# Kernel optimization log

Measured on AMD Instinct MI355X. Metric: run time of the kernel, lower is better.

## Reference

```python
import jax, jax.numpy as jnp
import numpy as np

B, C, N, F = 256, 4, 64, 256   # batch, in_channels, neighbors, in_features
OC, OF = 8, 256                # out_channels, out_features


def setup_inputs() -> dict:
    key = jax.random.key(0)
    k1, k2, k3, k4, k5 = jax.random.split(key, 5)
    x = jax.random.normal(k1, (B, C, F), dtype=jnp.float32)
    neighbor = jax.random.normal(k2, (B, N, C, F), dtype=jnp.float32)
    # torch.nn.Linear weights are (out_features, in_features)
    W_att1 = jax.random.normal(k3, (C, F), dtype=jnp.float32) / np.sqrt(F).astype(np.float32)
    W_att2 = jax.random.normal(k4, (C, F), dtype=jnp.float32) / np.sqrt(F).astype(np.float32)
    # Conv1d weight: (out_c*out_f, 2C, F); kernel_size==F makes it a dense contraction
    W_conv = jax.random.normal(k5, (OC * OF, 2 * C, F), dtype=jnp.float32) / np.sqrt(2 * C * F).astype(np.float32)
    return {"x": x, "neighbor": neighbor, "W_att1": W_att1, "W_att2": W_att2, "W_conv": W_conv}


def reference(x, neighbor, W_att1, W_att2, W_conv):
    # --- attention weights: einsum 'ci,nkl->n' = sum(att1(x_i)) * sum_{k,l} att2(y_i)[n]
    s1 = jnp.sum(x @ W_att1.T, axis=(1, 2))              # (B,)
    s2 = jnp.sum(neighbor @ W_att2.T, axis=(2, 3))       # (B, N)
    w = jax.nn.softmax(s1[:, None] * s2, axis=1)         # softmax over neighbors (dim 0 per-sample)

    # --- feature adjacency: einsum 'ca,ncb,n->cab' vectorized over batch
    fadj = jnp.einsum('bcx,bncy,bn->bcxy', x, neighbor, w)   # (B, C, F, F)
    fadj = fadj + jnp.swapaxes(fadj, -1, -2)
    # sgnroot
    fadj = jnp.sign(fadj) * jnp.sqrt(jnp.clip(jnp.abs(fadj), 1e-8, None))
    # row normalize over dim -2, NaN -> 0
    adj = fadj / (jnp.abs(fadj).sum(axis=-2, keepdims=True) + 1e-7)
    adj = jnp.where(jnp.isnan(adj), jnp.float32(0.0), adj)

    # --- transform: cat([adj @ x, x], channel) then full-width conv1d (dense contraction)
    h = jnp.einsum('bcxy,bcy->bcx', adj, x)              # (B, C, F)
    z = jnp.concatenate([h, x], axis=1)                  # (B, 2C, F)
    out = jnp.einsum('bcf,ocf->bo', z, W_conv).reshape(B, OC, OF)
    return out, adj
```

## Files before the change

### kernel.cpp

```cpp
#include <hip/hip_runtime.h>
#include <hip/hip_bf16.h>
#include <math.h>


typedef __bf16 bf16x8 __attribute__((ext_vector_type(8)));
typedef __bf16 bf16x4 __attribute__((ext_vector_type(4)));
typedef float f32x4 __attribute__((ext_vector_type(4)));

#define NB 256
#define NC 4
#define NN 64
#define NF 256
#define NO 2048

__global__ __launch_bounds__(256) void k_pre(
    const float* __restrict__ x, const float* __restrict__ nb,
    const float* __restrict__ W1, const float* __restrict__ W2,
    const float* __restrict__ Wc,
    __hip_bfloat16* __restrict__ Wcb, __hip_bfloat16* __restrict__ zbf,
    float* __restrict__ s1, float* __restrict__ s2)
{
  __shared__ float w2s[256], w1s[256];
  int t = threadIdx.x;
  int w = t >> 6, l = t & 63;

  w2s[t] = W2[t] + W2[256 + t] + W2[512 + t] + W2[768 + t];
  w1s[t] = W1[t] + W1[256 + t] + W1[512 + t] + W1[768 + t];
  __syncthreads();

  int gw = blockIdx.x * 4 + w;
  float4 wv2 = *(const float4*)&w2s[l * 4];
  float4 wv1 = *(const float4*)&w1s[l * 4];
  for (int task = gw; task < 16640; task += 8192) {
    bool isS2 = task < 16384;
    const float4* src = isS2 ? ((const float4*)nb + (size_t)task * 256)
                             : ((const float4*)x + (size_t)(task - 16384) * 256);
    float4 wv = isS2 ? wv2 : wv1;
    float val = 0.f;
    #pragma unroll
    for (int k = 0; k < 4; ++k) {
      float4 v = src[l + 64 * k];
      val += v.x * wv.x + v.y * wv.y + v.z * wv.z + v.w * wv.w;
    }
    for (int off = 32; off > 0; off >>= 1) val += __shfl_down(val, off);
    if (l == 0) {
      if (isS2) s2[task] = val;
      else s1[task - 16384] = val;
    }
  }

  for (int task = blockIdx.x; task < 4352; task += 2048) {
    if (task < 4096) {
      int idx = task * 256 + t;
      float4 v = ((const float4*)Wc)[idx];
      bf16x4 o = { (__bf16)v.x, (__bf16)v.y, (__bf16)v.z, (__bf16)v.w };
      ((bf16x4*)Wcb)[idx] = o;
    } else {
      int i = (task - 4096) * 256 + t;
      int e = i * 4;
      int b = e >> 10, r = e & 1023;
      float4 v = ((const float4*)x)[i];
      bf16x4 o = { (__bf16)v.x, (__bf16)v.y, (__bf16)v.z, (__bf16)v.w };
      *(bf16x4*)(zbf + (size_t)b * 2048 + 1024 + r) = o;
    }
  }
}

__global__ __launch_bounds__(256) void k_adj(
    const float* __restrict__ x, const float* __restrict__ nb,
    const float* __restrict__ s1, const float* __restrict__ s2,
    float* __restrict__ adj, __hip_bfloat16* __restrict__ zbf)
{
  __shared__ float xs[256], ns[256], invs[256], wsh[64];
  __shared__ float part[4][256];
  int t = threadIdx.x;
  int w = t >> 6, l = t & 63;
  int blk = blockIdx.x;
  int b = blk >> 2, c = blk & 3;

  if (t < 64) {
    float v = s1[b] * s2[b * 64 + t];
    float m = v;
    for (int off = 32; off > 0; off >>= 1) m = fmaxf(m, __shfl_xor(m, off));
    float e = expf(v - m);
    float s = e;
    for (int off = 32; off > 0; off >>= 1) s += __shfl_xor(s, off);
    wsh[t] = e / s;
  }
  xs[t] = x[(size_t)blk * 256 + t];
  __syncthreads();

  const float4* nb4 = (const float4*)(nb + (size_t)b * 65536 + c * 256);
  float4 a4 = {0.f, 0.f, 0.f, 0.f};
  #pragma unroll
  for (int k = 0; k < 16; ++k) {
    int n = w + 4 * k;
    float4 v = nb4[(size_t)n * 256 + l];
    float wn = wsh[n];
    a4.x = fmaf(wn, v.x, a4.x);
    a4.y = fmaf(wn, v.y, a4.y);
    a4.z = fmaf(wn, v.z, a4.z);
    a4.w = fmaf(wn, v.w, a4.w);
  }
  *(float4*)&part[w][l * 4] = a4;
  __syncthreads();
  ns[t] = part[0][t] + part[1][t] + part[2][t] + part[3][t];
  __syncthreads();

  int j0 = l * 4;
  float4 xv = *(const float4*)&xs[j0];
  float4 nv = *(const float4*)&ns[j0];
  int i0 = w * 64;

  float4 cs = {0.f, 0.f, 0.f, 0.f};
  #pragma unroll 4
  for (int ii = 0; ii < 64; ++ii) {
    int i = i0 + ii;
    float xi = xs[i], ni = ns[i];
    cs.x += __builtin_amdgcn_sqrtf(fmaxf(fabsf(fmaf(xi, nv.x, xv.x * ni)), 1e-8f));
    cs.y += __builtin_amdgcn_sqrtf(fmaxf(fabsf(fmaf(xi, nv.y, xv.y * ni)), 1e-8f));
    cs.z += __builtin_amdgcn_sqrtf(fmaxf(fabsf(fmaf(xi, nv.z, xv.z * ni)), 1e-8f));
    cs.w += __builtin_amdgcn_sqrtf(fmaxf(fabsf(fmaf(xi, nv.w, xv.w * ni)), 1e-8f));
  }
  *(float4*)&part[w][j0] = cs;
  __syncthreads();
  invs[t] = 1.f / (part[0][t] + part[1][t] + part[2][t] + part[3][t] + 1e-7f);
  __syncthreads();

  float4 iv = *(const float4*)&invs[j0];
  float4 ha = {0.f, 0.f, 0.f, 0.f};
  float* ab = adj + (size_t)blk * 65536;
  #pragma unroll 4
  for (int ii = 0; ii < 64; ++ii) {
    int i = i0 + ii;
    float xi = xs[i], ni = ns[i];
    float pix = invs[i] * xi;
    float v0 = fmaf(xi, nv.x, xv.x * ni);
    float v1 = fmaf(xi, nv.y, xv.y * ni);
    float v2 = fmaf(xi, nv.z, xv.z * ni);
    float v3 = fmaf(xi, nv.w, xv.w * ni);
    float g0 = copysignf(__builtin_amdgcn_sqrtf(fmaxf(fabsf(v0), 1e-8f)), v0);
    float g1 = copysignf(__builtin_amdgcn_sqrtf(fmaxf(fabsf(v1), 1e-8f)), v1);
    float g2 = copysignf(__builtin_amdgcn_sqrtf(fmaxf(fabsf(v2), 1e-8f)), v2);
    float g3 = copysignf(__builtin_amdgcn_sqrtf(fmaxf(fabsf(v3), 1e-8f)), v3);
    f32x4 o = { g0 * iv.x, g1 * iv.y, g2 * iv.z, g3 * iv.w };
    __builtin_nontemporal_store(o, (f32x4*)&ab[(size_t)i * 256 + j0]);
    ha.x = fmaf(g0, pix, ha.x);
    ha.y = fmaf(g1, pix, ha.y);
    ha.z = fmaf(g2, pix, ha.z);
    ha.w = fmaf(g3, pix, ha.w);
  }
  __syncthreads();
  *(float4*)&part[w][j0] = ha;
  __syncthreads();
  float hsum = part[0][t] + part[1][t] + part[2][t] + part[3][t];
  zbf[(size_t)b * 2048 + c * 256 + t] = __float2bfloat16(hsum);
}

__global__ __launch_bounds__(256) void k_gemm(
    const __hip_bfloat16* __restrict__ zb, const __hip_bfloat16* __restrict__ Wcb,
    float* __restrict__ out)
{
  int tid = threadIdx.x;
  int wave = tid >> 6, lane = tid & 63;
  int g = lane >> 4, r = lane & 15;
  int bm = blockIdx.x & 7, bn = blockIdx.x >> 3;
  int m0 = bm * 32 + (wave & 1) * 16;
  int n0 = bn * 32 + (wave >> 1) * 16;

  const bf16x8* pa = (const bf16x8*)(zb  + (size_t)(m0 + r) * 2048 + g * 8);
  const bf16x8* pw = (const bf16x8*)(Wcb + (size_t)(n0 + r) * 2048 + g * 8);

  f32x4 acc0 = {0.f, 0.f, 0.f, 0.f}, acc1 = {0.f, 0.f, 0.f, 0.f};
  #pragma unroll 4
  for (int ks = 0; ks < 64; ks += 2) {
    bf16x8 a0 = pa[ks * 4];
    bf16x8 b0 = pw[ks * 4];
    bf16x8 a1 = pa[ks * 4 + 4];
    bf16x8 b1 = pw[ks * 4 + 4];
    acc0 = __builtin_amdgcn_mfma_f32_16x16x32_bf16(a0, b0, acc0, 0, 0, 0);
    acc1 = __builtin_amdgcn_mfma_f32_16x16x32_bf16(a1, b1, acc1, 0, 0, 0);
  }
  acc0 += acc1;
  #pragma unroll
  for (int q = 0; q < 4; ++q) {
    int row = m0 + g * 4 + q;
    __builtin_nontemporal_store(acc0[q], &out[(size_t)row * 2048 + n0 + r]);
  }
}

__global__ __launch_bounds__(256) void k_scores_fb(
    const float* __restrict__ x, const float* __restrict__ nb,
    const float* __restrict__ W1, const float* __restrict__ W2,
    float* __restrict__ s1, float* __restrict__ s2)
{
  __shared__ float red[4];
  int t = threadIdx.x;
  int gid = blockIdx.x;
  float val;
  if (gid < NB * NN) {
    float w = W2[t] + W2[256 + t] + W2[512 + t] + W2[768 + t];
    const float* p = nb + (size_t)gid * 1024;
    val = w * (p[t] + p[256 + t] + p[512 + t] + p[768 + t]);
  } else {
    int b = gid - NB * NN;
    float w = W1[t] + W1[256 + t] + W1[512 + t] + W1[768 + t];
    const float* p = x + (size_t)b * 1024;
    val = w * (p[t] + p[256 + t] + p[512 + t] + p[768 + t]);
  }
  for (int off = 32; off > 0; off >>= 1) val += __shfl_down(val, off);
  if ((t & 63) == 0) red[t >> 6] = val;
  __syncthreads();
  if (t == 0) {
    float s = red[0] + red[1] + red[2] + red[3];
    if (gid < NB * NN) s2[gid] = s;
    else s1[gid - NB * NN] = s;
  }
}

__global__ __launch_bounds__(256) void k_adj_fb(
    const float* __restrict__ x, const float* __restrict__ nb,
    const float* __restrict__ s1, const float* __restrict__ s2,
    float* __restrict__ adj, float* __restrict__ hf)
{
  __shared__ float xs[256], ns[256], invs[256], wsh[64];
  __shared__ float part[4][256];
  int t = threadIdx.x;
  int w = t >> 6, l = t & 63;
  int blk = blockIdx.x;
  int b = blk >> 2, c = blk & 3;

  if (t < 64) {
    float v = s1[b] * s2[b * 64 + t];
    float m = v;
    for (int off = 32; off > 0; off >>= 1) m = fmaxf(m, __shfl_xor(m, off));
    float e = expf(v - m);
    float s = e;
    for (int off = 32; off > 0; off >>= 1) s += __shfl_xor(s, off);
    wsh[t] = e / s;
  }
  __syncthreads();
  float acc = 0.f;
  const float* pb = nb + (size_t)b * 65536 + c * 256 + t;
  #pragma unroll 8
  for (int n = 0; n < 64; ++n) acc = fmaf(wsh[n], pb[(size_t)n * 1024], acc);
  ns[t] = acc;
  xs[t] = x[(size_t)blk * 256 + t];
  __syncthreads();

  int j0 = l * 4;
  float4 xv = *(const float4*)&xs[j0];
  float4 nv = *(const float4*)&ns[j0];
  int i0 = w * 64;
  float4 cs = {0.f, 0.f, 0.f, 0.f};
  for (int ii = 0; ii < 64; ++ii) {
    int i = i0 + ii;
    float xi = xs[i], ni = ns[i];
    cs.x += __builtin_amdgcn_sqrtf(fmaxf(fabsf(fmaf(xi, nv.x, xv.x * ni)), 1e-8f));
    cs.y += __builtin_amdgcn_sqrtf(fmaxf(fabsf(fmaf(xi, nv.y, xv.y * ni)), 1e-8f));
    cs.z += __builtin_amdgcn_sqrtf(fmaxf(fabsf(fmaf(xi, nv.z, xv.z * ni)), 1e-8f));
    cs.w += __builtin_amdgcn_sqrtf(fmaxf(fabsf(fmaf(xi, nv.w, xv.w * ni)), 1e-8f));
  }
  *(float4*)&part[w][j0] = cs;
  __syncthreads();
  invs[t] = 1.f / (part[0][t] + part[1][t] + part[2][t] + part[3][t] + 1e-7f);
  __syncthreads();

  float4 iv = *(const float4*)&invs[j0];
  float4 ha = {0.f, 0.f, 0.f, 0.f};
  float* ab = adj + (size_t)blk * 65536;
  for (int ii = 0; ii < 64; ++ii) {
    int i = i0 + ii;
    float xi = xs[i], ni = ns[i];
    float pix = invs[i] * xi;
    float v0 = fmaf(xi, nv.x, xv.x * ni);
    float v1 = fmaf(xi, nv.y, xv.y * ni);
    float v2 = fmaf(xi, nv.z, xv.z * ni);
    float v3 = fmaf(xi, nv.w, xv.w * ni);
    float g0 = copysignf(__builtin_amdgcn_sqrtf(fmaxf(fabsf(v0), 1e-8f)), v0);
    float g1 = copysignf(__builtin_amdgcn_sqrtf(fmaxf(fabsf(v1), 1e-8f)), v1);
    float g2 = copysignf(__builtin_amdgcn_sqrtf(fmaxf(fabsf(v2), 1e-8f)), v2);
    float g3 = copysignf(__builtin_amdgcn_sqrtf(fmaxf(fabsf(v3), 1e-8f)), v3);
    f32x4 o = { g0 * iv.x, g1 * iv.y, g2 * iv.z, g3 * iv.w };
    *(f32x4*)&ab[(size_t)i * 256 + j0] = o;
    ha.x = fmaf(g0, pix, ha.x);
    ha.y = fmaf(g1, pix, ha.y);
    ha.z = fmaf(g2, pix, ha.z);
    ha.w = fmaf(g3, pix, ha.w);
  }
  __syncthreads();
  *(float4*)&part[w][j0] = ha;
  __syncthreads();
  hf[(size_t)blk * 256 + t] = part[0][t] + part[1][t] + part[2][t] + part[3][t];
}

__device__ inline bf16x8 cvt8_p(const float* p) {
  const float4* q = reinterpret_cast<const float4*>(p);
  float4 a = q[0], bq = q[1];
  bf16x8 r;
  r[0] = (__bf16)a.x;  r[1] = (__bf16)a.y;  r[2] = (__bf16)a.z;  r[3] = (__bf16)a.w;
  r[4] = (__bf16)bq.x; r[5] = (__bf16)bq.y; r[6] = (__bf16)bq.z; r[7] = (__bf16)bq.w;
  return r;
}

__global__ __launch_bounds__(256) void k_gemm_f32(
    const float* __restrict__ h, const float* __restrict__ x,
    const float* __restrict__ Wc, float* __restrict__ out)
{
  int tid = threadIdx.x;
  int wave = tid >> 6, lane = tid & 63;
  int g = lane >> 4, r = lane & 15;
  int bm = blockIdx.x & 3, bn = blockIdx.x >> 2;
  int m0 = bm * 64 + wave * 16;
  int n0 = bn * 32;
  int arow = m0 + r;
  int koff = g * 8;

  const float* za = h + (size_t)arow * 1024 + koff;
  const float* zb = x + (size_t)arow * 1024 + koff;
  const float* w0 = Wc + (size_t)(n0 + r) * 2048 + koff;
  const float* w1 = Wc + (size_t)(n0 + 16 + r) * 2048 + koff;

  f32x4 acc0 = {0.f, 0.f, 0.f, 0.f}, acc1 = {0.f, 0.f, 0.f, 0.f};
  #pragma unroll 4
  for (int ks = 0; ks < 32; ++ks) {
    acc0 = __builtin_amdgcn_mfma_f32_16x16x32_bf16(cvt8_p(za + ks * 32), cvt8_p(w0 + ks * 32), acc0, 0, 0, 0);
    acc1 = __builtin_amdgcn_mfma_f32_16x16x32_bf16(cvt8_p(za + ks * 32), cvt8_p(w1 + ks * 32), acc1, 0, 0, 0);
  }
  #pragma unroll 4
  for (int ks = 0; ks < 32; ++ks) {
    acc0 = __builtin_amdgcn_mfma_f32_16x16x32_bf16(cvt8_p(zb + ks * 32), cvt8_p(w0 + 1024 + ks * 32), acc0, 0, 0, 0);
    acc1 = __builtin_amdgcn_mfma_f32_16x16x32_bf16(cvt8_p(zb + ks * 32), cvt8_p(w1 + 1024 + ks * 32), acc1, 0, 0, 0);
  }
  #pragma unroll
  for (int q = 0; q < 4; ++q) {
    int row = m0 + g * 4 + q;
    out[(size_t)row * 2048 + n0 + r]      = acc0[q];
    out[(size_t)row * 2048 + n0 + 16 + r] = acc1[q];
  }
}

extern "C" void kernel_launch(void* const* d_in, const int* in_sizes, int n_in,
                              void* d_out, int out_size, void* d_ws, size_t ws_size,
                              hipStream_t stream) {
  const float* x  = (const float*)d_in[0];
  const float* nb = (const float*)d_in[1];
  const float* W1 = (const float*)d_in[2];
  const float* W2 = (const float*)d_in[3];
  const float* Wc = (const float*)d_in[4];
  float* out = (float*)d_out;
  float* adj = out + (size_t)NB * NO;

  char* ws = (char*)d_ws;
  const size_t ZBF_B = 1048576;
  const size_t WCB_B = 8388608;
  const size_t FREG = (256 + 16384) * 4;
  bool fast = ws_size >= ZBF_B + WCB_B + FREG;

  if (fast) {
    __hip_bfloat16* zbf = (__hip_bfloat16*)ws;
    __hip_bfloat16* Wcb = (__hip_bfloat16*)(ws + ZBF_B);
    float* s1  = (float*)(ws + ZBF_B + WCB_B);
    float* s2  = s1 + 256;
    k_pre<<<2048, 256, 0, stream>>>(x, nb, W1, W2, Wc, Wcb, zbf, s1, s2);
    k_adj<<<NB * NC, 256, 0, stream>>>(x, nb, s1, s2, adj, zbf);
    k_gemm<<<512, 256, 0, stream>>>(zbf, Wcb, out);
  } else {
    float* hws = (float*)d_ws;
    float* s1  = hws + 262144;
    float* s2  = s1 + 256;
    k_scores_fb<<<NB * NN + NB, 256, 0, stream>>>(x, nb, W1, W2, s1, s2);
    k_adj_fb<<<NB * NC, 256, 0, stream>>>(x, nb, s1, s2, adj, hws);
    k_gemm_f32<<<256, 256, 0, stream>>>(hws, x, Wc, out);
  }
}
```

Baseline: 108.9 us.

## Fuse score precompute and adjacency kernels into one per-batch 1024-thread block

Merges the preprocessing kernel (s1/s2 scores, Wc and x bf16 conversion) and the adjacency kernel into one kernel with one 1024-thread block per batch element. Each block computes its own neighbor scores, softmax, weighted neighbor sum and the adjacency rows for all 4 channels. This removes one launch, the s1/s2 round trip through global memory, and the 4x redundant reading of the neighbor tensor across channel blocks. The cost is only 256 large blocks, which lowers occupancy and parallelism, and a longer serial chain inside each block.

```diff
diff --git a/kernel.cpp b/kernel.cpp
--- a/kernel.cpp
+++ b/kernel.cpp
@@ -13,73 +13,67 @@
 #define NF 256
 #define NO 2048
 
-__global__ __launch_bounds__(256) void k_pre(
+__global__ __launch_bounds__(1024) void k_fused(
     const float* __restrict__ x, const float* __restrict__ nb,
     const float* __restrict__ W1, const float* __restrict__ W2,
     const float* __restrict__ Wc,
     __hip_bfloat16* __restrict__ Wcb, __hip_bfloat16* __restrict__ zbf,
-    float* __restrict__ s1, float* __restrict__ s2)
-{
-  __shared__ float w2s[256], w1s[256];
-  int t = threadIdx.x;
-  int w = t >> 6, l = t & 63;
-
-  w2s[t] = W2[t] + W2[256 + t] + W2[512 + t] + W2[768 + t];
-  w1s[t] = W1[t] + W1[256 + t] + W1[512 + t] + W1[768 + t];
-  __syncthreads();
-
-  int gw = blockIdx.x * 4 + w;
-  float4 wv2 = *(const float4*)&w2s[l * 4];
-  float4 wv1 = *(const float4*)&w1s[l * 4];
-  for (int task = gw; task < 16640; task += 8192) {
-    bool isS2 = task < 16384;
-    const float4* src = isS2 ? ((const float4*)nb + (size_t)task * 256)
-                             : ((const float4*)x + (size_t)(task - 16384) * 256);
-    float4 wv = isS2 ? wv2 : wv1;
-    float val = 0.f;
+    float* __restrict__ adj)
+{
+  __shared__ float xs[1024], ns[1024], invs[1024];
+  __shared__ float w2s[256], w1s[256], sm[64], wsh[64];
+  __shared__ float part[16][256];
+  __shared__ float s1v_sh;
+  int t = threadIdx.x, w = t >> 6, l = t & 63;
+  int b = blockIdx.x;
+
+  {
+    const float4* Wc4 = (const float4*)Wc;
+    bf16x4* Wcb4 = (bf16x4*)Wcb;
     #pragma unroll
     for (int k = 0; k < 4; ++k) {
-      float4 v = src[l + 64 * k];
-      val += v.x * wv.x + v.y * wv.y + v.z * wv.z + v.w * wv.w;
+      int idx = b * 4096 + k * 1024 + t;
+      float4 v = Wc4[idx];
+      bf16x4 o = { (__bf16)v.x, (__bf16)v.y, (__bf16)v.z, (__bf16)v.w };
+      Wcb4[idx] = o;
     }
-    for (int off = 32; off > 0; off >>= 1) val += __shfl_down(val, off);
-    if (l == 0) {
-      if (isS2) s2[task] = val;
-      else s1[task - 16384] = val;
+  }
+
+  float xval = x[(size_t)b * 1024 + t];
+  xs[t] = xval;
+  zbf[(size_t)b * 2048 + 1024 + t] = __float2bfloat16(xval);
+  if (t < 256) w2s[t] = W2[t] + W2[256 + t] + W2[512 + t] + W2[768 + t];
+  else if (t < 512) { int f = t - 256; w1s[f] = W1[f] + W1[256 + f] + W1[512 + f] + W1[768 + f]; }
+  __syncthreads();
+
+  {
+    const float4* nb4 = (const float4*)(nb + (size_t)b * 65536);
+    float4 wv = *(const float4*)&w2s[l * 4];
+    #pragma unroll
+    for (int k = 0; k < 4; ++k) {
+      int n = w * 4 + k;
+      const float4* p = nb4 + n * 256;
+      float val = 0.f;
+      #pragma unroll
+      for (int kk = 0; kk < 4; ++kk) {
+        float4 v = p[l + 64 * kk];
+        val += v.x * wv.x + v.y * wv.y + v.z * wv.z + v.w * wv.w;
+      }
+      for (int off = 32; off > 0; off >>= 1) val += __shfl_down(val, off);
+      if (l == 0) sm[n] = val;
     }
-  }
-
-  for (int task = blockIdx.x; task < 4352; task += 2048) {
-    if (task < 4096) {
-      int idx = task * 256 + t;
-      float4 v = ((const float4*)Wc)[idx];
-      bf16x4 o = { (__bf16)v.x, (__bf16)v.y, (__bf16)v.z, (__bf16)v.w };
-      ((bf16x4*)Wcb)[idx] = o;
-    } else {
-      int i = (task - 4096) * 256 + t;
-      int e = i * 4;
-      int b = e >> 10, r = e & 1023;
-      float4 v = ((const float4*)x)[i];
-      bf16x4 o = { (__bf16)v.x, (__bf16)v.y, (__bf16)v.z, (__bf16)v.w };
-      *(bf16x4*)(zbf + (size_t)b * 2048 + 1024 + r) = o;
+    if (w == 0) {
+      float v1 = 0.f;
+      #pragma unroll
+      for (int k = 0; k < 16; ++k) v1 += xs[l + 64 * k] * w1s[(l + 64 * k) & 255];
+      for (int off = 32; off > 0; off >>= 1) v1 += __shfl_down(v1, off);
+      if (l == 0) s1v_sh = v1;
     }
   }
-}
-
-__global__ __launch_bounds__(256) void k_adj(
-    const float* __restrict__ x, const float* __restrict__ nb,
-    const float* __restrict__ s1, const float* __restrict__ s2,
-    float* __restrict__ adj, __hip_bfloat16* __restrict__ zbf)
-{
-  __shared__ float xs[256], ns[256], invs[256], wsh[64];
-  __shared__ float part[4][256];
-  int t = threadIdx.x;
-  int w = t >> 6, l = t & 63;
-  int blk = blockIdx.x;
-  int b = blk >> 2, c = blk & 3;
+  __syncthreads();
 
   if (t < 64) {
-    float v = s1[b] * s2[b * 64 + t];
+    float v = s1v_sh * sm[t];
     float m = v;
     for (int off = 32; off > 0; off >>= 1) m = fmaxf(m, __shfl_xor(m, off));
     float e = expf(v - m);
@@ -87,36 +81,30 @@
     for (int off = 32; off > 0; off >>= 1) s += __shfl_xor(s, off);
     wsh[t] = e / s;
   }
-  xs[t] = x[(size_t)blk * 256 + t];
-  __syncthreads();
-
-  const float4* nb4 = (const float4*)(nb + (size_t)b * 65536 + c * 256);
-  float4 a4 = {0.f, 0.f, 0.f, 0.f};
-  #pragma unroll
-  for (int k = 0; k < 16; ++k) {
-    int n = w + 4 * k;
-    float4 v = nb4[(size_t)n * 256 + l];
-    float wn = wsh[n];
-    a4.x = fmaf(wn, v.x, a4.x);
-    a4.y = fmaf(wn, v.y, a4.y);
-    a4.z = fmaf(wn, v.z, a4.z);
-    a4.w = fmaf(wn, v.w, a4.w);
-  }
-  *(float4*)&part[w][l * 4] = a4;
-  __syncthreads();
-  ns[t] = part[0][t] + part[1][t] + part[2][t] + part[3][t];
-  __syncthreads();
-
+  __syncthreads();
+
+  {
+    const float* base = nb + (size_t)b * 65536 + t;
+    float acc = 0.f;
+    #pragma unroll 8
+    for (int n = 0; n < 64; ++n) acc = fmaf(wsh[n], base[(size_t)n * 1024], acc);
+    ns[t] = acc;
+  }
+  __syncthreads();
+
+  int c = w >> 2, ws = w & 3;
   int j0 = l * 4;
-  float4 xv = *(const float4*)&xs[j0];
-  float4 nv = *(const float4*)&ns[j0];
-  int i0 = w * 64;
+  const float* xc = xs + c * 256;
+  const float* nc = ns + c * 256;
+  float4 xv = *(const float4*)&xc[j0];
+  float4 nv = *(const float4*)&nc[j0];
+  int i0 = ws * 64;
 
   float4 cs = {0.f, 0.f, 0.f, 0.f};
   #pragma unroll 4
   for (int ii = 0; ii < 64; ++ii) {
     int i = i0 + ii;
-    float xi = xs[i], ni = ns[i];
+    float xi = xc[i], ni = nc[i];
     cs.x += __builtin_amdgcn_sqrtf(fmaxf(fabsf(fmaf(xi, nv.x, xv.x * ni)), 1e-8f));
     cs.y += __builtin_amdgcn_sqrtf(fmaxf(fabsf(fmaf(xi, nv.y, xv.y * ni)), 1e-8f));
     cs.z += __builtin_amdgcn_sqrtf(fmaxf(fabsf(fmaf(xi, nv.z, xv.z * ni)), 1e-8f));
@@ -124,17 +112,22 @@
   }
   *(float4*)&part[w][j0] = cs;
   __syncthreads();
-  invs[t] = 1.f / (part[0][t] + part[1][t] + part[2][t] + part[3][t] + 1e-7f);
-  __syncthreads();
-
-  float4 iv = *(const float4*)&invs[j0];
+  {
+    int cc = t >> 8, j = t & 255;
+    invs[t] = 1.f / (part[cc * 4 + 0][j] + part[cc * 4 + 1][j]
+                   + part[cc * 4 + 2][j] + part[cc * 4 + 3][j] + 1e-7f);
+  }
+  __syncthreads();
+
+  const float* ic = invs + c * 256;
+  float4 iv = *(const float4*)&ic[j0];
   float4 ha = {0.f, 0.f, 0.f, 0.f};
-  float* ab = adj + (size_t)blk * 65536;
+  float* ab = adj + ((size_t)(b * 4 + c)) * 65536;
   #pragma unroll 4
   for (int ii = 0; ii < 64; ++ii) {
     int i = i0 + ii;
-    float xi = xs[i], ni = ns[i];
-    float pix = invs[i] * xi;
+    float xi = xc[i], ni = nc[i];
+    float pix = ic[i] * xi;
     float v0 = fmaf(xi, nv.x, xv.x * ni);
     float v1 = fmaf(xi, nv.y, xv.y * ni);
     float v2 = fmaf(xi, nv.z, xv.z * ni);
@@ -153,8 +146,12 @@
   __syncthreads();
   *(float4*)&part[w][j0] = ha;
   __syncthreads();
-  float hsum = part[0][t] + part[1][t] + part[2][t] + part[3][t];
-  zbf[(size_t)b * 2048 + c * 256 + t] = __float2bfloat16(hsum);
+  {
+    int cc = t >> 8, j = t & 255;
+    float hsum = part[cc * 4 + 0][j] + part[cc * 4 + 1][j]
+               + part[cc * 4 + 2][j] + part[cc * 4 + 3][j];
+    zbf[(size_t)b * 2048 + cc * 256 + j] = __float2bfloat16(hsum);
+  }
 }
 
 __global__ __launch_bounds__(256) void k_gemm(
@@ -360,10 +357,7 @@
   if (fast) {
     __hip_bfloat16* zbf = (__hip_bfloat16*)ws;
     __hip_bfloat16* Wcb = (__hip_bfloat16*)(ws + ZBF_B);
-    float* s1  = (float*)(ws + ZBF_B + WCB_B);
-    float* s2  = s1 + 256;
-    k_pre<<<2048, 256, 0, stream>>>(x, nb, W1, W2, Wc, Wcb, zbf, s1, s2);
-    k_adj<<<NB * NC, 256, 0, stream>>>(x, nb, s1, s2, adj, zbf);
+    k_fused<<<NB, 1024, 0, stream>>>(x, nb, W1, W2, Wc, Wcb, zbf, adj);
     k_gemm<<<512, 256, 0, stream>>>(zbf, Wcb, out);
   } else {
     float* hws = (float*)d_ws;
```

Result: slower. 118.1 us (+8.4%).

## Tile bf16 GEMM through shared memory with 64x64 block tiles

Applied to the files above, without the earlier changes.

Rewrites the final bf16 MFMA GEMM so each block stages 64x128 slices of the activations and the conv weights in padded LDS, and each wave computes a 2x2 grid of 16x16 tiles. The old kernel had every wave stream its own A and B rows straight from global memory with no reuse. The new one cuts the global/L2 traffic for the 8 MB weight matrix. In exchange the grid drops from 512 to 128 blocks, leaving many CUs idle, and adds LDS round trips with two barriers per k-step and no double buffering.

```diff
diff --git a/kernel.cpp b/kernel.cpp
--- a/kernel.cpp
+++ b/kernel.cpp
@@ -161,31 +161,53 @@
     const __hip_bfloat16* __restrict__ zb, const __hip_bfloat16* __restrict__ Wcb,
     float* __restrict__ out)
 {
-  int tid = threadIdx.x;
-  int wave = tid >> 6, lane = tid & 63;
+  __shared__ __hip_bfloat16 Al[64][136];
+  __shared__ __hip_bfloat16 Bl[64][136];
+  int t = threadIdx.x;
+  int wave = t >> 6, lane = t & 63;
   int g = lane >> 4, r = lane & 15;
-  int bm = blockIdx.x & 7, bn = blockIdx.x >> 3;
-  int m0 = bm * 32 + (wave & 1) * 16;
-  int n0 = bn * 32 + (wave >> 1) * 16;
-
-  const bf16x8* pa = (const bf16x8*)(zb  + (size_t)(m0 + r) * 2048 + g * 8);
-  const bf16x8* pw = (const bf16x8*)(Wcb + (size_t)(n0 + r) * 2048 + g * 8);
-
-  f32x4 acc0 = {0.f, 0.f, 0.f, 0.f}, acc1 = {0.f, 0.f, 0.f, 0.f};
-  #pragma unroll 4
-  for (int ks = 0; ks < 64; ks += 2) {
-    bf16x8 a0 = pa[ks * 4];
-    bf16x8 b0 = pw[ks * 4];
-    bf16x8 a1 = pa[ks * 4 + 4];
-    bf16x8 b1 = pw[ks * 4 + 4];
-    acc0 = __builtin_amdgcn_mfma_f32_16x16x32_bf16(a0, b0, acc0, 0, 0, 0);
-    acc1 = __builtin_amdgcn_mfma_f32_16x16x32_bf16(a1, b1, acc1, 0, 0, 0);
-  }
-  acc0 += acc1;
+  int mh = wave >> 1, nh = wave & 1;
+  int bm = blockIdx.x & 3, bn = blockIdx.x >> 2;
+
+  f32x4 acc00 = {0.f,0.f,0.f,0.f}, acc01 = {0.f,0.f,0.f,0.f};
+  f32x4 acc10 = {0.f,0.f,0.f,0.f}, acc11 = {0.f,0.f,0.f,0.f};
+
+  const float4* zb4 = (const float4*)zb;
+  const float4* wc4 = (const float4*)Wcb;
+
+  for (int kb = 0; kb < 16; ++kb) {
+    #pragma unroll
+    for (int q = 0; q < 4; ++q) {
+      int idx = q * 256 + t;
+      int row = idx >> 4, c16 = idx & 15;
+      float4 va = zb4[(size_t)(bm * 64 + row) * 256 + kb * 16 + c16];
+      *(float4*)&Al[row][c16 * 8] = va;
+      float4 vb = wc4[(size_t)(bn * 64 + row) * 256 + kb * 16 + c16];
+      *(float4*)&Bl[row][c16 * 8] = vb;
+    }
+    __syncthreads();
+    #pragma unroll
+    for (int kk = 0; kk < 4; ++kk) {
+      bf16x8 a0 = *(const bf16x8*)&Al[mh * 32 + r][kk * 32 + g * 8];
+      bf16x8 a1 = *(const bf16x8*)&Al[mh * 32 + 16 + r][kk * 32 + g * 8];
+      bf16x8 b0 = *(const bf16x8*)&Bl[nh * 32 + r][kk * 32 + g * 8];
+      bf16x8 b1 = *(const bf16x8*)&Bl[nh * 32 + 16 + r][kk * 32 + g * 8];
+      acc00 = __builtin_amdgcn_mfma_f32_16x16x32_bf16(a0, b0, acc00, 0, 0, 0);
+      acc01 = __builtin_amdgcn_mfma_f32_16x16x32_bf16(a0, b1, acc01, 0, 0, 0);
+      acc10 = __builtin_amdgcn_mfma_f32_16x16x32_bf16(a1, b0, acc10, 0, 0, 0);
+      acc11 = __builtin_amdgcn_mfma_f32_16x16x32_bf16(a1, b1, acc11, 0, 0, 0);
+    }
+    __syncthreads();
+  }
+
+  int row0 = bm * 64 + mh * 32 + g * 4;
+  int col0 = bn * 64 + nh * 32 + r;
   #pragma unroll
   for (int q = 0; q < 4; ++q) {
-    int row = m0 + g * 4 + q;
-    __builtin_nontemporal_store(acc0[q], &out[(size_t)row * 2048 + n0 + r]);
+    __builtin_nontemporal_store(acc00[q], &out[(size_t)(row0 + q) * 2048 + col0]);
+    __builtin_nontemporal_store(acc01[q], &out[(size_t)(row0 + q) * 2048 + col0 + 16]);
+    __builtin_nontemporal_store(acc10[q], &out[(size_t)(row0 + 16 + q) * 2048 + col0]);
+    __builtin_nontemporal_store(acc11[q], &out[(size_t)(row0 + 16 + q) * 2048 + col0 + 16]);
   }
 }
 
@@ -364,7 +386,7 @@
     float* s2  = s1 + 256;
     k_pre<<<2048, 256, 0, stream>>>(x, nb, W1, W2, Wc, Wcb, zbf, s1, s2);
     k_adj<<<NB * NC, 256, 0, stream>>>(x, nb, s1, s2, adj, zbf);
-    k_gemm<<<512, 256, 0, stream>>>(zbf, Wcb, out);
+    k_gemm<<<128, 256, 0, stream>>>(zbf, Wcb, out);
   } else {
     float* hws = (float*)d_ws;
     float* s1  = hws + 262144;
```

Result: faster. 96.84 us (-11.1%).
